# Performance work log

Measured on AMD Instinct MI355X. Metric: run time of the kernel, lower is better.

Reference implementation:

```python
import jax, jax.numpy as jnp
import numpy as np

B_, L_, D_ = 8, 2048, 1024      # batch, seq_len, d_model
E, DS, K = 2, 16, 4             # expand, d_state, d_conv
DI = E * D_                     # d_inner = 2048
DTR = (D_ + 15) // 16           # dt_rank = 64


def setup_inputs() -> dict:
    key = jax.random.key(0)
    ks = jax.random.split(key, 8)
    g = lambda k, sh, sc=0.02: jax.random.normal(k, sh, jnp.float32) * sc
    return {
        "x": jax.random.normal(ks[0], (B_, L_, D_), jnp.float32),
        "ln_w": jnp.ones((D_,), jnp.float32),
        "ln_b": jnp.zeros((D_,), jnp.float32),
        "W_in": g(ks[1], (D_, 2 * DI)),
        "conv_w": g(ks[2], (DI, 1, K), 0.1),
        "conv_b": jnp.zeros((DI,), jnp.float32),
        "W_x": g(ks[3], (DI, DTR + 2 * DS)),
        "W_dt": g(ks[4], (DTR, DI), 0.1),
        "b_dt": jnp.full((DI,), -4.0, jnp.float32),  # softplus(-4) ~ 0.018 (small init dt)
        "A_log": jnp.log(jnp.broadcast_to(jnp.arange(1, DS + 1, dtype=jnp.float32), (DI, DS))),
        "Dp": jnp.ones((DI,), jnp.float32),
        "W_out": g(ks[5], (DI, D_)),
    }


def _mamba_block(x, ln_w, ln_b, W_in, conv_w, conv_b, W_x, W_dt, b_dt, A_log, Dp, W_out):
    # pre-norm
    mu = jnp.mean(x, axis=-1, keepdims=True)
    var = jnp.var(x, axis=-1, keepdims=True)
    xn = (x - mu) / jnp.sqrt(var + 1e-5) * ln_w + ln_b

    # input projection -> (u, z), each (B, L, DI)
    xz = jnp.einsum('bld,de->ble', xn, W_in)
    u, z = jnp.split(xz, 2, axis=-1)

    # causal depthwise conv1d along L
    uc = jax.lax.conv_general_dilated(
        u.transpose(0, 2, 1), conv_w, window_strides=(1,), padding=[(K - 1, 0)],
        feature_group_count=DI, dimension_numbers=('NCH', 'OIH', 'NCH'))
    u = jax.nn.silu(uc.transpose(0, 2, 1) + conv_b)

    # input-dependent SSM params
    xd = jnp.einsum('bld,de->ble', u, W_x)          # (B, L, DTR + 2*DS)
    dt = jax.nn.softplus(jnp.einsum('blr,rd->bld', xd[..., :DTR], W_dt) + b_dt)  # (B, L, DI)
    Bm = xd[..., DTR:DTR + DS]                       # (B, L, DS)
    Cm = xd[..., DTR + DS:]                          # (B, L, DS)
    A = -jnp.exp(A_log)                              # (DI, DS)

    # selective scan over time; carry h: (B, DI, DS)
    def step(h, inp):
        dt_t, u_t, B_t, C_t = inp                    # (B,DI),(B,DI),(B,DS),(B,DS)
        dA = jnp.exp(dt_t[..., None] * A)            # (B, DI, DS)
        h = h * dA + (dt_t * u_t)[..., None] * B_t[:, None, :]
        y = jnp.einsum('bds,bs->bd', h, C_t)
        return h, y

    h0 = jnp.zeros((x.shape[0], DI, DS), x.dtype)
    xs = (dt.transpose(1, 0, 2), u.transpose(1, 0, 2), Bm.transpose(1, 0, 2), Cm.transpose(1, 0, 2))
    _, ys = jax.lax.scan(step, h0, xs)               # ys: (L, B, DI)

    y = ys.transpose(1, 0, 2) + u * Dp
    y = y * jax.nn.silu(z)
    # output projection + residual (dropout is identity in eval)
    return jnp.einsum('bld,de->ble', y, W_out) + x


def reference(x, ln_w, ln_b, W_in, conv_w, conv_b, W_x, W_dt, b_dt, A_log, Dp, W_out):
    return _mamba_block(x, ln_w, ln_b, W_in, conv_w, conv_b, W_x, W_dt, b_dt, A_log, Dp, W_out)
```

## Files before the change

### kernel.cpp

```cpp
#include <hip/hip_runtime.h>

#define NB 8
#define NL 2048
#define ND 1024
#define NDI 2048
#define NDS 16
#define NDTR 64
#define NM (NB * NL)
#define CH 16
#define CL (NL / CH)

__device__ __forceinline__ float bf2f(unsigned int u) {
  union { unsigned int i; float f; } c; c.i = u << 16; return c.f;
}
__device__ __forceinline__ float lo16(unsigned int w) { return __uint_as_float(w << 16); }
__device__ __forceinline__ float hi16(unsigned int w) { return __uint_as_float(w & 0xffff0000u); }
__device__ __forceinline__ unsigned short f2bf(float f) {
  unsigned int x = __float_as_uint(f);
  x = x + 0x7fffu + ((x >> 16) & 1u);
  return (unsigned short)(x >> 16);
}
__device__ __forceinline__ void dec8(int4 raw, float* f) {
  f[0] = lo16((unsigned)raw.x); f[1] = hi16((unsigned)raw.x);
  f[2] = lo16((unsigned)raw.y); f[3] = hi16((unsigned)raw.y);
  f[4] = lo16((unsigned)raw.z); f[5] = hi16((unsigned)raw.z);
  f[6] = lo16((unsigned)raw.w); f[7] = hi16((unsigned)raw.w);
}
__device__ __forceinline__ float softplus_fast(float x) {
  return fmaxf(x, 0.f) + __logf(1.f + __expf(-fabsf(x)));
}

typedef __bf16 bf16x8 __attribute__((ext_vector_type(8)));
typedef float f32x4 __attribute__((ext_vector_type(4)));

__device__ __forceinline__ void gld_lds16(const unsigned short* g, unsigned short* l) {
  __builtin_amdgcn_global_load_lds(
      (const __attribute__((address_space(1))) unsigned int*)g,
      (__attribute__((address_space(3))) unsigned int*)l, 16, 0, 0);
}

__global__ __launch_bounds__(256) void k_ln(const float* __restrict__ x,
    const float* __restrict__ lw, const float* __restrict__ lb,
    unsigned short* __restrict__ xn)
{
  const int row = blockIdx.x;
  const int tid = threadIdx.x;
  const float* xr = x + (size_t)row * ND;
  float4 v = reinterpret_cast<const float4*>(xr)[tid];
  float s  = v.x + v.y + v.z + v.w;
  float s2 = v.x*v.x + v.y*v.y + v.z*v.z + v.w*v.w;
  #pragma unroll
  for (int m = 32; m >= 1; m >>= 1) {
    s  += __shfl_xor(s, m);
    s2 += __shfl_xor(s2, m);
  }
  __shared__ float red[8];
  const int wid = tid >> 6;
  if ((tid & 63) == 0) { red[wid] = s; red[4 + wid] = s2; }
  __syncthreads();
  s  = red[0] + red[1] + red[2] + red[3];
  s2 = red[4] + red[5] + red[6] + red[7];
  const float mu   = s * (1.0f / ND);
  const float var  = s2 * (1.0f / ND) - mu * mu;
  const float rstd = rsqrtf(var + 1e-5f);
  const float4 wv = reinterpret_cast<const float4*>(lw)[tid];
  const float4 bv = reinterpret_cast<const float4*>(lb)[tid];
  ushort4 o;
  o.x = f2bf((v.x - mu) * rstd * wv.x + bv.x);
  o.y = f2bf((v.y - mu) * rstd * wv.y + bv.y);
  o.z = f2bf((v.z - mu) * rstd * wv.z + bv.z);
  o.w = f2bf((v.w - mu) * rstd * wv.w + bv.w);
  reinterpret_cast<ushort4*>(xn + (size_t)row * ND)[tid] = o;
}

__global__ __launch_bounds__(256) void k_transpose(
    const float* __restrict__ W, unsigned short* __restrict__ WT,
    const int K, const int N)
{
  __shared__ float t[32][33];
  const int k0 = blockIdx.y * 32, n0 = blockIdx.x * 32;
  const int tx = threadIdx.x & 31, ty = threadIdx.x >> 5;
  #pragma unroll
  for (int r = 0; r < 4; ++r)
    t[ty + r * 8][tx] = W[(size_t)(k0 + ty + r * 8) * N + n0 + tx];
  __syncthreads();
  #pragma unroll
  for (int r = 0; r < 4; ++r)
    WT[(size_t)(n0 + ty + r * 8) * K + k0 + tx] = f2bf(t[tx][ty + r * 8]);
}

template<int MODE>
__global__ __launch_bounds__(512, 2) void k_mfma8(
    const unsigned short* __restrict__ A, const unsigned short* __restrict__ BT,
    const int K, const int N, void* __restrict__ O0, void* __restrict__ O1,
    const float* __restrict__ aux)
{
  __shared__ __align__(16) unsigned short sh[65536];
  const int tid = threadIdx.x, lane = tid & 63, wv = tid >> 6;
  const int wm = wv >> 2, wn = wv & 3;
  const int m16 = lane & 15, kb = lane >> 4;
  const int swzs = (((kb * 16) ^ (((m16 >> 1) & 3) << 4)) >> 1);
  const int arow = wm * 128 + m16;
  const int brow = wn * 64 + m16;

  int wg = blockIdx.x;
  const int cpx = gridDim.x >> 3;
  wg = (wg & 7) * cpx + (wg >> 3);
  const int gnx = N >> 8;
  const int m0 = (wg / gnx) << 8;
  const int n0 = (wg % gnx) << 8;

  f32x4 acc[8][4];
  #pragma unroll
  for (int i = 0; i < 8; ++i)
    #pragma unroll
    for (int j = 0; j < 4; ++j)
      #pragma unroll
      for (int r = 0; r < 4; ++r) acc[i][j][r] = 0.f;

  auto STAGE = [&](const unsigned short* X, int x0, int kg, unsigned short* base) {
    #pragma unroll
    for (int jj = 0; jj < 2; ++jj) {
      const int s = (wv * 2 + jj) * 64 + lane;
      const int row = s >> 2;
      const int c = (lane & 3) ^ ((row >> 1) & 3);
      gld_lds16(X + (size_t)(x0 + row) * K + kg + c * 8, base + (wv * 2 + jj) * 512);
    }
  };
  auto RD_A = [&](bf16x8* dst, const unsigned short* base, int FH) {
    #pragma unroll
    for (int i = 0; i < 4; ++i)
      dst[i] = *reinterpret_cast<const bf16x8*>(base + (arow + FH * 64 + i * 16) * 32 + swzs);
  };
  auto RD_B = [&](bf16x8* dst, const unsigned short* base) {
    #pragma unroll
    for (int j = 0; j < 4; ++j)
      dst[j] = *reinterpret_cast<const bf16x8*>(base + (brow + j * 16) * 32 + swzs);
  };
  auto MM = [&](const bf16x8* aF, const bf16x8* bF, int off) {
    #pragma unroll
    for (int i = 0; i < 4; ++i)
      #pragma unroll
      for (int j = 0; j < 4; ++j)
        acc[off + i][j] = __builtin_amdgcn_mfma_f32_16x16x32_bf16(aF[i], bF[j], acc[off + i][j], 0, 0, 0);
  };

  STAGE(A,  m0, 0,  sh);
  STAGE(BT, n0, 0,  sh + 32768);
  STAGE(A,  m0, 32, sh + 8192);
  STAGE(BT, n0, 32, sh + 32768 + 8192);
  asm volatile("s_waitcnt vmcnt(0)" ::: "memory");
  __builtin_amdgcn_s_barrier();

  bf16x8 aA[4], aB[4], bA[4], bB[4];
  RD_A(aA, sh, 0);
  RD_B(bA, sh + 32768);

  const int NT = K >> 6;
  for (int t = 0; t < NT; ++t) {
    const int buf = t & 1, nb = buf ^ 1;
    const int kn = (t << 6) + 64;
    const bool more = (t + 1 < NT);
    const unsigned short* cA = sh + buf * 16384;
    const unsigned short* cB = sh + 32768 + buf * 16384;
    unsigned short* nA = sh + nb * 16384;
    unsigned short* nB = sh + 32768 + nb * 16384;

    if (more) { STAGE(A, m0, kn, nA); STAGE(BT, n0, kn, nB); }
    RD_A(aB, cA, 1);
    __builtin_amdgcn_sched_barrier(0);
    __builtin_amdgcn_s_setprio(1); MM(aA, bA, 0); __builtin_amdgcn_s_setprio(0);
    __builtin_amdgcn_s_barrier();

    if (more) { STAGE(A, m0, kn + 32, nA + 8192); STAGE(BT, n0, kn + 32, nB + 8192); }
    if (more) { asm volatile("s_waitcnt vmcnt(8)" ::: "memory"); }
    else      { asm volatile("s_waitcnt vmcnt(0)" ::: "memory"); }
    __builtin_amdgcn_s_barrier();
    RD_A(aA, cA + 8192, 0);
    RD_B(bB, cB + 8192);
    __builtin_amdgcn_sched_barrier(0);
    __builtin_amdgcn_s_setprio(1); MM(aB, bA, 4); __builtin_amdgcn_s_setprio(0);
    __builtin_amdgcn_s_barrier();

    RD_A(aB, cA + 8192, 1);
    __builtin_amdgcn_sched_barrier(0);
    __builtin_amdgcn_s_setprio(1); MM(aA, bB, 0); __builtin_amdgcn_s_setprio(0);
    __builtin_amdgcn_s_barrier();

    if (more) asm volatile("s_waitcnt vmcnt(4)" ::: "memory");
    __builtin_amdgcn_s_barrier();
    if (more) { RD_A(aA, nA, 0); RD_B(bA, nB); }
    __builtin_amdgcn_sched_barrier(0);
    __builtin_amdgcn_s_setprio(1); MM(aB, bB, 4); __builtin_amdgcn_s_setprio(0);
    __builtin_amdgcn_s_barrier();
  }

  {
    float* fsh = (float*)sh;
    constexpr int LDP = 260;
    const int erow = tid >> 4;
    const int ec0  = tid & 15;
    const int growb = m0 + (erow >> 4) * 128 + (erow & 15);
    #pragma unroll
    for (int i = 0; i < 8; ++i) {
      __builtin_amdgcn_s_barrier();
      #pragma unroll
      for (int j = 0; j < 4; ++j)
        #pragma unroll
        for (int r = 0; r < 4; ++r)
          fsh[(wm * 16 + kb * 4 + r) * LDP + wn * 64 + j * 16 + m16] = acc[i][j][r];
      __builtin_amdgcn_s_barrier();
      const int grow = growb + i * 16;
      #pragma unroll
      for (int q = 0; q < 4; ++q) {
        const int c = (ec0 + q * 16) * 4;
        float4 v = *reinterpret_cast<const float4*>(&fsh[erow * LDP + c]);
        const int colg = n0 + c;
        if constexpr (MODE == 0) {
          ushort4 o = {f2bf(v.x), f2bf(v.y), f2bf(v.z), f2bf(v.w)};
          unsigned short* dst = (colg < NDI)
              ? (unsigned short*)O0 + (size_t)grow * NDI + colg
              : (unsigned short*)O1 + (size_t)grow * NDI + colg - NDI;
          *reinterpret_cast<ushort4*>(dst) = o;
        } else {
          float4 rv = *reinterpret_cast<const float4*>(aux + (size_t)grow * N + colg);
          float4 o = {v.x + rv.x, v.y + rv.y, v.z + rv.z, v.w + rv.w};
          *reinterpret_cast<float4*>((float*)O0 + (size_t)grow * N + colg) = o;
        }
      }
    }
  }
  (void)O1; (void)aux;
}

__global__ __launch_bounds__(256) void k_mfma_dt(
    const unsigned short* __restrict__ A, const unsigned short* __restrict__ BT,
    const int K, void* __restrict__ O0, const float* __restrict__ aux, const int N)
{
  __shared__ __align__(16) unsigned short As[128 * 32];
  __shared__ __align__(16) unsigned short Bs[128 * 32];
  const int tid = threadIdx.x;
  const int lane = tid & 63;
  const int wv = tid >> 6;
  const int wm = wv >> 1, wn = wv & 1;
  const int m0 = blockIdx.y * 128, n0 = blockIdx.x * 128;
  const int m16 = lane & 15, kb = lane >> 4;
  const int wbase = wv * 64;

  f32x4 acc[4][4];
  #pragma unroll
  for (int i = 0; i < 4; ++i)
    #pragma unroll
    for (int j = 0; j < 4; ++j)
      #pragma unroll
      for (int r = 0; r < 4; ++r) acc[i][j][r] = 0.f;

  for (int k0 = 0; k0 < K; k0 += 32) {
    #pragma unroll
    for (int it = 0; it < 2; ++it) {
      const int c = it * 256 + tid;
      const int r = c >> 2, cb = c & 3;
      gld_lds16(A  + (size_t)(m0 + r) * K + k0 + cb * 8, As + (size_t)(it * 256 + wbase) * 8);
      gld_lds16(BT + (size_t)(n0 + r) * K + k0 + cb * 8, Bs + (size_t)(it * 256 + wbase) * 8);
    }
    __syncthreads();
    bf16x8 af[4], bfr[4];
    #pragma unroll
    for (int i = 0; i < 4; ++i)
      af[i] = *reinterpret_cast<const bf16x8*>(&As[(wm * 64 + i * 16 + m16) * 32 + kb * 8]);
    #pragma unroll
    for (int j = 0; j < 4; ++j)
      bfr[j] = *reinterpret_cast<const bf16x8*>(&Bs[(wn * 64 + j * 16 + m16) * 32 + kb * 8]);
    #pragma unroll
    for (int i = 0; i < 4; ++i)
      #pragma unroll
      for (int j = 0; j < 4; ++j)
        acc[i][j] = __builtin_amdgcn_mfma_f32_16x16x32_bf16(af[i], bfr[j], acc[i][j], 0, 0, 0);
    __syncthreads();
  }

  const int r0 = (lane >> 4) * 4;
  #pragma unroll
  for (int i = 0; i < 4; ++i) {
    const int rowb = m0 + wm * 64 + i * 16 + r0;
    #pragma unroll
    for (int j = 0; j < 4; ++j) {
      const int col = n0 + wn * 64 + j * 16 + m16;
      #pragma unroll
      for (int r = 0; r < 4; ++r) {
        const int row = rowb + r;
        ((unsigned short*)O0)[(size_t)row * N + col] =
            f2bf(softplus_fast(acc[i][j][r] + aux[col]));
      }
    }
  }
}

__global__ __launch_bounds__(256) void k_conv(
    const unsigned short* __restrict__ up, const float* __restrict__ cw,
    const float* __restrict__ cb, unsigned short* __restrict__ u)
{
  const int tid = threadIdx.x;
  const int c0 = tid * 8;
  const int lt = blockIdx.x & 127;
  const int b  = blockIdx.x >> 7;
  const int l0 = lt * 16;

  float4 wv[8];
  #pragma unroll
  for (int j = 0; j < 8; ++j)
    wv[j] = reinterpret_cast<const float4*>(cw + (size_t)c0 * 4)[j];
  float bias[8];
  {
    float4 b0 = reinterpret_cast<const float4*>(cb + c0)[0];
    float4 b1 = reinterpret_cast<const float4*>(cb + c0)[1];
    bias[0]=b0.x; bias[1]=b0.y; bias[2]=b0.z; bias[3]=b0.w;
    bias[4]=b1.x; bias[5]=b1.y; bias[6]=b1.z; bias[7]=b1.w;
  }

  const size_t base = ((size_t)b * NL + l0) * NDI + c0;
  float w0[8], w1[8], w2[8];
  if (l0 >= 3) {
    int4 r0 = *reinterpret_cast<const int4*>(up + base - 3 * NDI);
    int4 r1 = *reinterpret_cast<const int4*>(up + base - 2 * NDI);
    int4 r2 = *reinterpret_cast<const int4*>(up + base - 1 * NDI);
    dec8(r0, w0); dec8(r1, w1); dec8(r2, w2);
  } else {
    #pragma unroll
    for (int j = 0; j < 8; ++j) { w0[j] = 0.f; w1[j] = 0.f; w2[j] = 0.f; }
  }

  #pragma unroll
  for (int l = 0; l < 16; ++l) {
    int4 raw = *reinterpret_cast<const int4*>(up + base + (size_t)l * NDI);
    float cur[8];
    dec8(raw, cur);
    unsigned short o[8];
    #pragma unroll
    for (int j = 0; j < 8; ++j) {
      const float a = bias[j] + wv[j].x * w0[j] + wv[j].y * w1[j]
                              + wv[j].z * w2[j] + wv[j].w * cur[j];
      o[j] = f2bf(a / (1.f + __expf(-a)));
    }
    ushort4 o0 = {o[0], o[1], o[2], o[3]};
    ushort4 o1 = {o[4], o[5], o[6], o[7]};
    unsigned short* dst = u + base + (size_t)l * NDI;
    *reinterpret_cast<ushort4*>(dst)     = o0;
    *reinterpret_cast<ushort4*>(dst + 4) = o1;
    #pragma unroll
    for (int j = 0; j < 8; ++j) { w0[j] = w1[j]; w1[j] = w2[j]; w2[j] = cur[j]; }
  }
}

__global__ __launch_bounds__(256) void k_xd_mfma(
    const unsigned short* __restrict__ A, const unsigned short* __restrict__ BT,
    unsigned short* __restrict__ xdt, float* __restrict__ xb,
    float* __restrict__ xc)
{
  __shared__ __align__(16) unsigned short As[2][64 * 32];
  __shared__ __align__(16) unsigned short Bs[2][96 * 32];
  const int tid = threadIdx.x, lane = tid & 63, wvv = tid >> 6;
  const int m0 = blockIdx.x * 64;
  const int m16 = lane & 15, kb = lane >> 4;
  const int sw = (kb ^ ((m16 >> 1) & 3)) * 8;

  f32x4 acc[6];
  #pragma unroll
  for (int j = 0; j < 6; ++j)
    #pragma unroll
    for (int r = 0; r < 4; ++r) acc[j][r] = 0.f;

  auto STG = [&](int bb, int kg) {
    {
      const int row = tid >> 2, c = tid & 3;
      const int sc = c ^ ((row >> 1) & 3);
      gld_lds16(A + (size_t)(m0 + row) * NDI + kg + sc * 8, &As[bb][tid * 8]);
      gld_lds16(BT + (size_t)row * NDI + kg + sc * 8, &Bs[bb][tid * 8]);
    }
    if (tid < 128) {
      const int s = 256 + tid;
      const int row = s >> 2, c = s & 3;
      const int sc = c ^ ((row >> 1) & 3);
      gld_lds16(BT + (size_t)row * NDI + kg + sc * 8, &Bs[bb][s * 8]);
    }
  };

  STG(0, 0);
  asm volatile("s_waitcnt vmcnt(0)" ::: "memory");
  __syncthreads();

  for (int t = 0; t < NDI / 32; ++t) {
    const int cur = t & 1;
    if (t + 1 < NDI / 32) STG(cur ^ 1, (t + 1) * 32);
    bf16x8 af = *reinterpret_cast<const bf16x8*>(&As[cur][(wvv * 16 + m16) * 32 + sw]);
    bf16x8 bfr[6];
    #pragma unroll
    for (int j = 0; j < 6; ++j)
      bfr[j] = *reinterpret_cast<const bf16x8*>(&Bs[cur][(j * 16 + m16) * 32 + sw]);
    #pragma unroll
    for (int j = 0; j < 6; ++j)
      acc[j] = __builtin_amdgcn_mfma_f32_16x16x32_bf16(af, bfr[j], acc[j], 0, 0, 0);
    asm volatile("s_waitcnt vmcnt(0)" ::: "memory");
    __syncthreads();
  }

  const int r0 = kb * 4;
  #pragma unroll
  for (int j = 0; j < 6; ++j) {
    const int col = j * 16 + m16;
    #pragma unroll
    for (int r = 0; r < 4; ++r) {
      const int row = m0 + wvv * 16 + r0 + r;
      const float v = acc[j][r];
      if (j < 4)       xdt[(size_t)row * 64 + col] = f2bf(v);
      else if (j == 4) xb[(size_t)row * 16 + col - 64] = v;
      else             xc[(size_t)row * 16 + col - 80] = v;
    }
  }
}

template<int PHASE>
__global__ __launch_bounds__(256) void k_scan3(
    const unsigned short* __restrict__ dt, unsigned short* __restrict__ u_io,
    const unsigned short* __restrict__ z,
    const float* __restrict__ xb, const float* __restrict__ xc,
    const float* __restrict__ A_log, const float* __restrict__ Dp,
    float* __restrict__ HF, float* __restrict__ Sdt)
{
  const int tid = threadIdx.x;
  const int blk = blockIdx.x;
  const int b = blk >> 7;
  const int c = (blk >> 3) & (CH - 1);
  if (PHASE == 0 && c == CH - 1) return;
  const int d = (blk & 7) * 256 + tid;

  __shared__ float Bsl[CL][16];
  __shared__ float Csl[(PHASE == 1) ? CL : 1][16];
  const size_t rbase = (size_t)b * NL + (size_t)c * CL;
  #pragma unroll
  for (int i = 0; i < 2; ++i) {
    const int idx = i * 256 + tid;
    const int r = idx >> 2, q = idx & 3;
    reinterpret_cast<float4*>(&Bsl[r][q * 4])[0] =
        reinterpret_cast<const float4*>(xb + (rbase + r) * 16)[q];
    if constexpr (PHASE == 1)
      reinterpret_cast<float4*>(&Csl[r][q * 4])[0] =
          reinterpret_cast<const float4*>(xc + (rbase + r) * 16)[q];
  }
  __syncthreads();

  float Ac[16];
  #pragma unroll
  for (int q = 0; q < 4; ++q) {
    float4 a = reinterpret_cast<const float4*>(A_log + (size_t)d * 16)[q];
    Ac[q*4+0] = -__expf(a.x); Ac[q*4+1] = -__expf(a.y);
    Ac[q*4+2] = -__expf(a.z); Ac[q*4+3] = -__expf(a.w);
  }
  bool fastok = true;
  #pragma unroll
  for (int s = 1; s < 16; ++s)
    fastok = fastok && (fabsf(Ac[s] - Ac[0] * (float)(s + 1)) <= 1e-5f * fabsf(Ac[s]));
  const bool fast = __all(fastok);

  const size_t hoff = ((size_t)(b * CH + c) * NDI + d) * 16;
  float h[16];
  if constexpr (PHASE == 0) {
    #pragma unroll
    for (int s = 0; s < 16; ++s) h[s] = 0.f;
  } else {
    #pragma unroll
    for (int q = 0; q < 4; ++q) {
      float4 hv = reinterpret_cast<const float4*>(HF + hoff)[q];
      h[q*4+0] = hv.x; h[q*4+1] = hv.y; h[q*4+2] = hv.z; h[q*4+3] = hv.w;
    }
  }
  const float Dd = Dp[d];
  const float Ac0 = Ac[0];
  float sdt = 0.f;
  size_t idx = rbase * NDI + d;

  if (fast) {
    for (int l = 0; l < CL; ++l, idx += NDI) {
      const float dtv = bf2f(dt[idx]);
      const float uv  = bf2f(u_io[idx]);
      const float dtu = dtv * uv;
      const float qq = __expf(dtv * Ac0);
      float e = qq;
      if constexpr (PHASE == 0) {
        sdt += dtv;
        #pragma unroll
        for (int s = 0; s < 16; ++s) {
          h[s] = h[s] * e + dtu * Bsl[l][s];
          e *= qq;
        }
      } else {
        float yp = 0.f;
        #pragma unroll
        for (int s = 0; s < 16; ++s) {
          h[s] = h[s] * e + dtu * Bsl[l][s];
          yp += h[s] * Csl[l][s];
          e *= qq;
        }
        const float zv = bf2f(z[idx]);
        const float sil = zv / (1.f + __expf(-zv));
        u_io[idx] = f2bf((yp + uv * Dd) * sil);
      }
    }
  } else {
    for (int l = 0; l < CL; ++l, idx += NDI) {
      const float dtv = bf2f(dt[idx]);
      const float uv  = bf2f(u_io[idx]);
      const float dtu = dtv * uv;
      if constexpr (PHASE == 0) {
        sdt += dtv;
        #pragma unroll
        for (int s = 0; s < 16; ++s) {
          const float e = __expf(dtv * Ac[s]);
          h[s] = h[s] * e + dtu * Bsl[l][s];
        }
      } else {
        float yp = 0.f;
        #pragma unroll
        for (int s = 0; s < 16; ++s) {
          const float e = __expf(dtv * Ac[s]);
          h[s] = h[s] * e + dtu * Bsl[l][s];
          yp += h[s] * Csl[l][s];
        }
        const float zv = bf2f(z[idx]);
        const float sil = zv / (1.f + __expf(-zv));
        u_io[idx] = f2bf((yp + uv * Dd) * sil);
      }
    }
  }

  if constexpr (PHASE == 0) {
    #pragma unroll
    for (int q = 0; q < 4; ++q) {
      float4 hv = {h[q*4+0], h[q*4+1], h[q*4+2], h[q*4+3]};
      reinterpret_cast<float4*>(HF + hoff)[q] = hv;
    }
    Sdt[(size_t)(b * CH + c) * NDI + d] = sdt;
  }
}

__global__ __launch_bounds__(256) void k_comb(
    float* __restrict__ HF, const float* __restrict__ Sdt,
    const float* __restrict__ A_log)
{
  const int t = blockIdx.x * 256 + threadIdx.x;
  const int b = t >> 15;
  const int q = t & 32767;
  const int d = q >> 4;
  const float Ac = -__expf(A_log[q]);
  float H = 0.f;
  #pragma unroll
  for (int c = 0; c < CH; ++c) {
    const size_t off = (((size_t)(b * CH + c) * NDI) << 4) + q;
    const float hf = HF[off];
    const float p  = __expf(Ac * Sdt[(size_t)(b * CH + c) * NDI + d]);
    HF[off] = H;
    H = p * H + hf;
  }
}

extern "C" void kernel_launch(void* const* d_in, const int* in_sizes, int n_in,
                              void* d_out, int out_size, void* d_ws, size_t ws_size,
                              hipStream_t stream) {
  (void)in_sizes; (void)n_in; (void)out_size; (void)ws_size;
  const float* x      = (const float*)d_in[0];
  const float* ln_w   = (const float*)d_in[1];
  const float* ln_b   = (const float*)d_in[2];
  const float* W_in   = (const float*)d_in[3];
  const float* conv_w = (const float*)d_in[4];
  const float* conv_b = (const float*)d_in[5];
  const float* W_x    = (const float*)d_in[6];
  const float* W_dt   = (const float*)d_in[7];
  const float* b_dt   = (const float*)d_in[8];
  const float* A_log  = (const float*)d_in[9];
  const float* Dp     = (const float*)d_in[10];
  const float* W_out  = (const float*)d_in[11];
  float* out = (float*)d_out;

  char* ws = (char*)d_ws;
  unsigned short* xn   = (unsigned short*)(ws);
  float*          HF   = (float*)(ws);
  unsigned short* upre = (unsigned short*)(ws + 33554432);
  unsigned short* zbuf = (unsigned short*)(ws + 100663296);
  unsigned short* ubuf = (unsigned short*)(ws + 167772160);
  unsigned short* xdt  = (unsigned short*)(ws + 234881024);
  float*          Sdt  = (float*)(ws + 234881024);
  float*          xb   = (float*)(ws + 236978176);
  float*          xc   = (float*)(ws + 238026752);
  unsigned short* WxT  = (unsigned short*)(ws + 239075328);
  unsigned short* WdtT = (unsigned short*)(ws + 239468544);
  unsigned short* WinT = (unsigned short*)(ws + 240123904);
  unsigned short* WoutT= (unsigned short*)(ws + 248512512);

  dim3 gt1(4096 / 32, 1024 / 32);
  k_transpose<<<gt1, 256, 0, stream>>>(W_in, WinT, 1024, 4096);
  dim3 gt2(1024 / 32, 2048 / 32);
  k_transpose<<<gt2, 256, 0, stream>>>(W_out, WoutT, 2048, 1024);
  dim3 gt3(96 / 32, 2048 / 32);
  k_transpose<<<gt3, 256, 0, stream>>>(W_x, WxT, 2048, 96);
  dim3 gt4(2048 / 32, 64 / 32);
  k_transpose<<<gt4, 256, 0, stream>>>(W_dt, WdtT, 64, 2048);

  k_ln<<<NM, 256, 0, stream>>>(x, ln_w, ln_b, xn);

  k_mfma8<0><<<(NM / 256) * (4096 / 256), 512, 0, stream>>>(
      xn, WinT, 1024, 4096, upre, zbuf, nullptr);

  k_conv<<<NB * (NL / 16), 256, 0, stream>>>(upre, conv_w, conv_b, ubuf);

  k_xd_mfma<<<NM / 64, 256, 0, stream>>>(ubuf, WxT, xdt, xb, xc);

  dim3 g3(2048 / 128, NM / 128);
  k_mfma_dt<<<g3, 256, 0, stream>>>(xdt, WdtT, 64, upre, b_dt, 2048);

  const int nscan = NB * CH * (NDI / 256);
  k_scan3<0><<<nscan, 256, 0, stream>>>(upre, ubuf, zbuf, xb, xc, A_log, Dp, HF, Sdt);
  k_comb<<<NB * NDI * NDS / 256, 256, 0, stream>>>(HF, Sdt, A_log);
  k_scan3<1><<<nscan, 256, 0, stream>>>(upre, ubuf, zbuf, xb, xc, A_log, Dp, HF, Sdt);

  k_mfma8<1><<<(NM / 256) * (1024 / 256), 512, 0, stream>>>(
      ubuf, WoutT, 2048, 1024, out, nullptr, x);
}
```

Before: 548.4 us.

## Replace 8-phase GEMM pipeline with simple double-buffered 32-wide K loop

Rewrites the bf16 MFMA GEMM main loop. The old version used a 128KB LDS, 64-wide K step, interleaved 4-phase schedule. The new one uses a 64KB LDS double buffer with a 32-wide K step, one prefetch per iteration and a single vmcnt(0) wait plus barrier. This halves LDS use and removes many barriers, but exposes global-load latency more because each tile's loads must finish before the next iteration.

```diff
diff --git a/kernel.cpp b/kernel.cpp
--- a/kernel.cpp
+++ b/kernel.cpp
@@ -90,12 +90,12 @@
 }
 
 template<int MODE>
-__global__ __launch_bounds__(512, 2) void k_mfma8(
+__global__ __launch_bounds__(512, 2) void k_mfma2(
     const unsigned short* __restrict__ A, const unsigned short* __restrict__ BT,
     const int K, const int N, void* __restrict__ O0, void* __restrict__ O1,
     const float* __restrict__ aux)
 {
-  __shared__ __align__(16) unsigned short sh[65536];
+  __shared__ __align__(16) unsigned short sh[32768];
   const int tid = threadIdx.x, lane = tid & 63, wv = tid >> 6;
   const int wm = wv >> 2, wn = wv & 3;
   const int m16 = lane & 15, kb = lane >> 4;
@@ -145,53 +145,33 @@
         acc[off + i][j] = __builtin_amdgcn_mfma_f32_16x16x32_bf16(aF[i], bF[j], acc[off + i][j], 0, 0, 0);
   };
 
-  STAGE(A,  m0, 0,  sh);
-  STAGE(BT, n0, 0,  sh + 32768);
-  STAGE(A,  m0, 32, sh + 8192);
-  STAGE(BT, n0, 32, sh + 32768 + 8192);
+  STAGE(A,  m0, 0, sh);
+  STAGE(BT, n0, 0, sh + 8192);
   asm volatile("s_waitcnt vmcnt(0)" ::: "memory");
   __builtin_amdgcn_s_barrier();
 
-  bf16x8 aA[4], aB[4], bA[4], bB[4];
-  RD_A(aA, sh, 0);
-  RD_B(bA, sh + 32768);
-
-  const int NT = K >> 6;
+  const int NT = K >> 5;
   for (int t = 0; t < NT; ++t) {
-    const int buf = t & 1, nb = buf ^ 1;
-    const int kn = (t << 6) + 64;
+    const int buf = t & 1;
+    const unsigned short* cA = sh + buf * 16384;
+    const unsigned short* cB = cA + 8192;
+    unsigned short* nA = sh + (buf ^ 1) * 16384;
     const bool more = (t + 1 < NT);
-    const unsigned short* cA = sh + buf * 16384;
-    const unsigned short* cB = sh + 32768 + buf * 16384;
-    unsigned short* nA = sh + nb * 16384;
-    unsigned short* nB = sh + 32768 + nb * 16384;
-
-    if (more) { STAGE(A, m0, kn, nA); STAGE(BT, n0, kn, nB); }
-    RD_A(aB, cA, 1);
+    if (more) {
+      const int kn = (t + 1) << 5;
+      STAGE(A,  m0, kn, nA);
+      STAGE(BT, n0, kn, nA + 8192);
+    }
+    bf16x8 a0[4], a1[4], bF[4];
+    RD_A(a0, cA, 0);
+    RD_B(bF, cB);
+    RD_A(a1, cA, 1);
     __builtin_amdgcn_sched_barrier(0);
-    __builtin_amdgcn_s_setprio(1); MM(aA, bA, 0); __builtin_amdgcn_s_setprio(0);
-    __builtin_amdgcn_s_barrier();
-
-    if (more) { STAGE(A, m0, kn + 32, nA + 8192); STAGE(BT, n0, kn + 32, nB + 8192); }
-    if (more) { asm volatile("s_waitcnt vmcnt(8)" ::: "memory"); }
-    else      { asm volatile("s_waitcnt vmcnt(0)" ::: "memory"); }
-    __builtin_amdgcn_s_barrier();
-    RD_A(aA, cA + 8192, 0);
-    RD_B(bB, cB + 8192);
-    __builtin_amdgcn_sched_barrier(0);
-    __builtin_amdgcn_s_setprio(1); MM(aB, bA, 4); __builtin_amdgcn_s_setprio(0);
-    __builtin_amdgcn_s_barrier();
-
-    RD_A(aB, cA + 8192, 1);
-    __builtin_amdgcn_sched_barrier(0);
-    __builtin_amdgcn_s_setprio(1); MM(aA, bB, 0); __builtin_amdgcn_s_setprio(0);
-    __builtin_amdgcn_s_barrier();
-
-    if (more) asm volatile("s_waitcnt vmcnt(4)" ::: "memory");
-    __builtin_amdgcn_s_barrier();
-    if (more) { RD_A(aA, nA, 0); RD_B(bA, nB); }
-    __builtin_amdgcn_sched_barrier(0);
-    __builtin_amdgcn_s_setprio(1); MM(aB, bB, 4); __builtin_amdgcn_s_setprio(0);
+    __builtin_amdgcn_s_setprio(1);
+    MM(a0, bF, 0);
+    MM(a1, bF, 4);
+    __builtin_amdgcn_s_setprio(0);
+    if (more) asm volatile("s_waitcnt vmcnt(0)" ::: "memory");
     __builtin_amdgcn_s_barrier();
   }
 
@@ -607,7 +587,7 @@
 
   k_ln<<<NM, 256, 0, stream>>>(x, ln_w, ln_b, xn);
 
-  k_mfma8<0><<<(NM / 256) * (4096 / 256), 512, 0, stream>>>(
+  k_mfma2<0><<<(NM / 256) * (4096 / 256), 512, 0, stream>>>(
       xn, WinT, 1024, 4096, upre, zbuf, nullptr);
 
   k_conv<<<NB * (NL / 16), 256, 0, stream>>>(upre, conv_w, conv_b, ubuf);
@@ -622,6 +602,6 @@
   k_comb<<<NB * NDI * NDS / 256, 256, 0, stream>>>(HF, Sdt, A_log);
   k_scan3<1><<<nscan, 256, 0, stream>>>(upre, ubuf, zbuf, xb, xc, A_log, Dp, HF, Sdt);
 
-  k_mfma8<1><<<(NM / 256) * (1024 / 256), 512, 0, stream>>>(
+  k_mfma2<1><<<(NM / 256) * (1024 / 256), 512, 0, stream>>>(
       ubuf, WoutT, 2048, 1024, out, nullptr, x);
 }
```

Result: no change. 540.8 us (-1.4%).
